# Kernel optimization log

Measured on AMD Instinct MI355X. Metric: run time of the kernel, lower is better.

Reference implementation:

```python
import jax, jax.numpy as jnp
import numpy as np

EXPR_MASK_RATIO = 0.4
POS_MASK_RATIO = 0.33
MIN_VISIBLE_GENES = 10


def setup_inputs() -> dict:
    key = jax.random.key(0)
    k1, k2 = jax.random.split(key)
    expression = jax.random.normal(k1, (16, 1024, 2000), dtype=jnp.float32)
    position = jax.random.normal(k2, (16, 1024, 3), dtype=jnp.float32)
    return {"expression": expression, "position": position}


def _expression_mask(expression, key):
    # strategy == 'random': rand matrix, kthvalue threshold, mask = rand >= threshold
    B, N, G = expression.shape
    num_masked = max(1, int(G * EXPR_MASK_RATIO))
    num_masked = min(num_masked, G - MIN_VISIBLE_GENES)
    rand = jax.random.uniform(key, (B, N, G), dtype=jnp.float32)
    # torch.kthvalue(rand, G - num_masked): (G - num_masked)-th smallest value,
    # i.e. index G - num_masked - 1 of the ascending sort (keepdim=True).
    kth = jnp.sort(rand, axis=-1)[..., G - num_masked - 1 : G - num_masked]  # (B,N,1)
    return rand >= kth  # bool (B,N,G); includes the threshold element, as in torch code


def _position_mask(position, key):
    # Vectorized form of the per-(b,n) loop:
    #   r < ratio*0.3      -> mask 2 of 3 dims (randperm(3)[:2] == complement of one uniform dim)
    #   ratio*0.3 <= r < ratio -> mask 1 uniform dim
    B, N, _ = position.shape
    kr, k1, k2 = jax.random.split(key, 3)
    r = jax.random.uniform(kr, (B, N), dtype=jnp.float32)
    two = r < POS_MASK_RATIO * 0.3
    one = (r < POS_MASK_RATIO) & (~two)
    dim1 = jax.random.randint(k1, (B, N), 0, 3)  # dim masked in the 1-dim branch
    excl = jax.random.randint(k2, (B, N), 0, 3)  # dim kept in the 2-dim branch
    eye = jnp.eye(3, dtype=bool)
    m1 = eye[dim1]        # (B,N,3) one-hot
    m2 = ~eye[excl]       # (B,N,3) two hot
    false3 = jnp.zeros((B, N, 3), dtype=bool)
    return jnp.where(two[..., None], m2, jnp.where(one[..., None], m1, false3))


def reference(expression, position):
    key = jax.random.key(42)
    ke, kp = jax.random.split(key)
    expr_mask = _expression_mask(expression, ke)   # (B,N,G) bool
    pos_mask = _position_mask(position, kp)        # (B,N,3) bool
    return expr_mask, pos_mask
```

## Files before the change

### kernel.cpp

```cpp
#include <hip/hip_runtime.h>
#include <stdint.h>

#define TF_ROUND(x0, x1, r)                    \
  {                                            \
    x0 += x1;                                  \
    x1 = (x1 << (r)) | (x1 >> (32 - (r)));     \
    x1 ^= x0;                                  \
  }

__host__ __device__ inline void threefry2x32(uint32_t k0, uint32_t k1,
                                             uint32_t x0, uint32_t x1,
                                             uint32_t& o0, uint32_t& o1) {
  const uint32_t ks2 = k0 ^ k1 ^ 0x1BD11BDAu;
  x0 += k0; x1 += k1;
  TF_ROUND(x0, x1, 13) TF_ROUND(x0, x1, 15) TF_ROUND(x0, x1, 26) TF_ROUND(x0, x1, 6)
  x0 += k1; x1 += ks2 + 1u;
  TF_ROUND(x0, x1, 17) TF_ROUND(x0, x1, 29) TF_ROUND(x0, x1, 16) TF_ROUND(x0, x1, 24)
  x0 += ks2; x1 += k0 + 2u;
  TF_ROUND(x0, x1, 13) TF_ROUND(x0, x1, 15) TF_ROUND(x0, x1, 26) TF_ROUND(x0, x1, 6)
  x0 += k0; x1 += k1 + 3u;
  TF_ROUND(x0, x1, 17) TF_ROUND(x0, x1, 29) TF_ROUND(x0, x1, 16) TF_ROUND(x0, x1, 24)
  x0 += k1; x1 += ks2 + 4u;
  TF_ROUND(x0, x1, 13) TF_ROUND(x0, x1, 15) TF_ROUND(x0, x1, 26) TF_ROUND(x0, x1, 6)
  x0 += ks2; x1 += k0 + 5u;
  o0 = x0; o1 = x1;
}

__device__ inline uint32_t random_bits32(uint32_t k0, uint32_t k1, uint32_t i) {
  uint32_t y0, y1;
  threefry2x32(k0, k1, 0u, i, y0, y1);
  return y0 ^ y1;
}

constexpr int B = 16;
constexpr int N = 1024;
constexpr int G = 2000;
constexpr int NUM_ROWS = B * N;
constexpr uint32_t RANK = (uint32_t)(G - 800 - 1);
constexpr long long EXPR_ELEMS = (long long)NUM_ROWS * G;
constexpr int PER_THREAD = 8;
constexpr int ACTIVE_T = G / PER_THREAD;

typedef int v4i __attribute__((ext_vector_type(4)));

__global__ __launch_bounds__(256) void fused_mask_kernel(
    int32_t* __restrict__ out_expr, int32_t* __restrict__ out_pos,
    uint32_t ke0, uint32_t ke1,
    uint32_t kr0, uint32_t kr1,
    uint32_t ah0, uint32_t ah1, uint32_t al0, uint32_t al1,
    uint32_t bh0, uint32_t bh1, uint32_t bl0, uint32_t bl1) {
  __shared__ alignas(16) uint32_t hist[256];
  __shared__ uint32_t cand[256];
  __shared__ uint32_t s_posbits[5];
  __shared__ uint32_t s_cnt;
  __shared__ uint32_t s_bucket;
  __shared__ uint32_t s_kk;
  __shared__ uint32_t s_thr;

  const int t = threadIdx.x;
  const uint32_t row = blockIdx.x;
  const uint32_t base = row * (uint32_t)G + (uint32_t)t * (uint32_t)PER_THREAD;
  const bool active = (t < ACTIVE_T);

  hist[t] = 0u;
  if (t == 0) s_cnt = 0u;
  __syncthreads();

  uint32_t m[PER_THREAD];
  if (active) {
#pragma unroll
    for (int j = 0; j < PER_THREAD; ++j) {
      uint32_t bits = random_bits32(ke0, ke1, base + (uint32_t)j);
      m[j] = bits >> 9;
      atomicAdd(&hist[m[j] >> 15], 1u);
    }
  } else if (t < 255) {
    uint32_t pk0, pk1;
    switch (t) {
      case 250: pk0 = kr0; pk1 = kr1; break;
      case 251: pk0 = ah0; pk1 = ah1; break;
      case 252: pk0 = al0; pk1 = al1; break;
      case 253: pk0 = bh0; pk1 = bh1; break;
      default:  pk0 = bl0; pk1 = bl1; break;
    }
    s_posbits[t - 250] = random_bits32(pk0, pk1, row);
  }
  __syncthreads();

  if (t < 64) {
    uint4 h = reinterpret_cast<const uint4*>(hist)[t];
    uint32_t tot = h.x + h.y + h.z + h.w;
    uint32_t x = tot;
#pragma unroll
    for (int d = 1; d < 64; d <<= 1) {
      uint32_t o = __shfl_up(x, d, 64);
      if (t >= d) x += o;
    }
    uint32_t e0 = x - tot;
    uint32_t e1 = e0 + h.x;
    uint32_t e2 = e1 + h.y;
    uint32_t e3 = e2 + h.z;
    if (e0 <= RANK && RANK < e1) { s_bucket = 4u * t + 0u; s_kk = RANK - e0; }
    if (e1 <= RANK && RANK < e2) { s_bucket = 4u * t + 1u; s_kk = RANK - e1; }
    if (e2 <= RANK && RANK < e3) { s_bucket = 4u * t + 2u; s_kk = RANK - e2; }
    if (e3 <= RANK && RANK < e3 + h.w) { s_bucket = 4u * t + 3u; s_kk = RANK - e3; }
  } else if (t == 255) {
    uint32_t rb = s_posbits[0];
    union { uint32_t u; float f; } cvt;
    cvt.u = (rb >> 9) | 0x3F800000u;
    float r = cvt.f - 1.0f;
    const float THR2 = (float)(0.33 * 0.3);
    const float THR1 = (float)0.33;
    bool two = r < THR2;
    bool one = (r < THR1) && !two;
    int dim1 = (int)(((s_posbits[1] % 3u) + (s_posbits[2] % 3u)) % 3u);
    int excl = (int)(((s_posbits[3] % 3u) + (s_posbits[4] % 3u)) % 3u);
    uint32_t obase = row * 3u;
#pragma unroll
    for (int d = 0; d < 3; ++d) {
      bool mval = two ? (d != excl) : (one ? (d == dim1) : false);
      out_pos[obase + (uint32_t)d] = mval ? 1 : 0;
    }
  }
  __syncthreads();

  const uint32_t bucket = s_bucket;
  if (active) {
#pragma unroll
    for (int j = 0; j < PER_THREAD; ++j) {
      if ((m[j] >> 15) == bucket) {
        uint32_t p = atomicAdd(&s_cnt, 1u);
        if (p < 256u) cand[p] = m[j];
      }
    }
  }
  __syncthreads();

  const uint32_t c = (s_cnt < 256u) ? s_cnt : 256u;
  const uint32_t kk = s_kk;
  if ((uint32_t)t < c) {
    uint32_t mv = cand[t];
    uint32_t r = 0;
    for (uint32_t j = 0; j < c; ++j) {
      uint32_t mj = cand[j];
      r += (mj < mv) || (mj == mv && j < (uint32_t)t);
    }
    if (r == kk) s_thr = mv;
  }
  __syncthreads();

  const uint32_t thr = s_thr;
  if (active) {
    v4i a, b;
    a.x = (m[0] >= thr) ? 1 : 0;
    a.y = (m[1] >= thr) ? 1 : 0;
    a.z = (m[2] >= thr) ? 1 : 0;
    a.w = (m[3] >= thr) ? 1 : 0;
    b.x = (m[4] >= thr) ? 1 : 0;
    b.y = (m[5] >= thr) ? 1 : 0;
    b.z = (m[6] >= thr) ? 1 : 0;
    b.w = (m[7] >= thr) ? 1 : 0;
    v4i* p = (v4i*)(out_expr + base);
    __builtin_nontemporal_store(a, p);
    __builtin_nontemporal_store(b, p + 1);
  }
}

extern "C" void kernel_launch(void* const* d_in, const int* in_sizes, int n_in,
                              void* d_out, int out_size, void* d_ws, size_t ws_size,
                              hipStream_t stream) {
  (void)d_in; (void)in_sizes; (void)n_in; (void)d_ws; (void)ws_size; (void)out_size;

  uint32_t ke0, ke1, kp0, kp1;
  threefry2x32(0u, 42u, 0u, 0u, ke0, ke1);
  threefry2x32(0u, 42u, 0u, 1u, kp0, kp1);
  uint32_t kr0, kr1, ka0, ka1, kb0, kb1;
  threefry2x32(kp0, kp1, 0u, 0u, kr0, kr1);
  threefry2x32(kp0, kp1, 0u, 1u, ka0, ka1);
  threefry2x32(kp0, kp1, 0u, 2u, kb0, kb1);
  uint32_t ah0, ah1, al0, al1, bh0, bh1, bl0, bl1;
  threefry2x32(ka0, ka1, 0u, 0u, ah0, ah1);
  threefry2x32(ka0, ka1, 0u, 1u, al0, al1);
  threefry2x32(kb0, kb1, 0u, 0u, bh0, bh1);
  threefry2x32(kb0, kb1, 0u, 1u, bl0, bl1);

  int32_t* out_expr = (int32_t*)d_out;
  int32_t* out_pos = out_expr + EXPR_ELEMS;

  fused_mask_kernel<<<NUM_ROWS, 256, 0, stream>>>(
      out_expr, out_pos, ke0, ke1, kr0, kr1,
      ah0, ah1, al0, al1, bh0, bh1, bl0, bl1);
}
```

Baseline: 244.1 us.

## Process one row per wavefront with wave-level selection and 4-wide threefry

Each 64-lane wavefront now handles a whole row, 32 elements per lane, so a block covers four rows. Block-wide __syncthreads are replaced with wave barriers, shuffles and ballots for the histogram scan, candidate ranking and threshold broadcast. Threefry is computed four counters at a time with alignbit rotates, and stores become coalesced 16-byte chunks strided by 256 elements. The cost is much higher register pressure from m[32], which may lower occupancy, and the candidate buffer is capped at 64 entries.

```diff
diff --git a/kernel.cpp b/kernel.cpp
--- a/kernel.cpp
+++ b/kernel.cpp
@@ -26,10 +26,34 @@
   o0 = x0; o1 = x1;
 }
 
-__device__ inline uint32_t random_bits32(uint32_t k0, uint32_t k1, uint32_t i) {
-  uint32_t y0, y1;
-  threefry2x32(k0, k1, 0u, i, y0, y1);
-  return y0 ^ y1;
+#define RND4(r)                                                     \
+  _Pragma("unroll") for (int e = 0; e < 4; ++e) {                   \
+    x0[e] += x1[e];                                                 \
+    x1[e] = __builtin_amdgcn_alignbit(x1[e], x1[e], 32u - (r));     \
+    x1[e] ^= x0[e];                                                 \
+  }
+#define INJ4(a, b)                                                  \
+  _Pragma("unroll") for (int e = 0; e < 4; ++e) {                   \
+    x0[e] += (a);                                                   \
+    x1[e] += (b);                                                   \
+  }
+
+__device__ __forceinline__ void tf4(uint32_t k0, uint32_t k1, uint32_t ks2,
+                                    uint32_t tbk, uint32_t lit, uint32_t out[4]) {
+  uint32_t x0[4], x1[4];
+#pragma unroll
+  for (int e = 0; e < 4; ++e) { x0[e] = k0; x1[e] = tbk + (lit + (uint32_t)e); }
+  RND4(13) RND4(15) RND4(26) RND4(6)
+  INJ4(k1, ks2 + 1u)
+  RND4(17) RND4(29) RND4(16) RND4(24)
+  INJ4(ks2, k0 + 2u)
+  RND4(13) RND4(15) RND4(26) RND4(6)
+  INJ4(k0, k1 + 3u)
+  RND4(17) RND4(29) RND4(16) RND4(24)
+  INJ4(k1, ks2 + 4u)
+  RND4(13) RND4(15) RND4(26) RND4(6)
+#pragma unroll
+  for (int e = 0; e < 4; ++e) out[e] = (x0[e] + ks2) ^ (x1[e] + (k0 + 5u));
 }
 
 constexpr int B = 16;
@@ -38,8 +62,7 @@
 constexpr int NUM_ROWS = B * N;
 constexpr uint32_t RANK = (uint32_t)(G - 800 - 1);
 constexpr long long EXPR_ELEMS = (long long)NUM_ROWS * G;
-constexpr int PER_THREAD = 8;
-constexpr int ACTIVE_T = G / PER_THREAD;
+constexpr int ROWS_PER_BLOCK = 4;
 
 typedef int v4i __attribute__((ext_vector_type(4)));
 
@@ -49,120 +72,149 @@
     uint32_t kr0, uint32_t kr1,
     uint32_t ah0, uint32_t ah1, uint32_t al0, uint32_t al1,
     uint32_t bh0, uint32_t bh1, uint32_t bl0, uint32_t bl1) {
-  __shared__ alignas(16) uint32_t hist[256];
-  __shared__ uint32_t cand[256];
-  __shared__ uint32_t s_posbits[5];
-  __shared__ uint32_t s_cnt;
-  __shared__ uint32_t s_bucket;
-  __shared__ uint32_t s_kk;
-  __shared__ uint32_t s_thr;
+  __shared__ alignas(16) uint32_t hist[ROWS_PER_BLOCK][256];
+  __shared__ uint32_t cand[ROWS_PER_BLOCK][64];
+  __shared__ uint32_t cnt[ROWS_PER_BLOCK];
 
   const int t = threadIdx.x;
-  const uint32_t row = blockIdx.x;
-  const uint32_t base = row * (uint32_t)G + (uint32_t)t * (uint32_t)PER_THREAD;
-  const bool active = (t < ACTIVE_T);
-
-  hist[t] = 0u;
-  if (t == 0) s_cnt = 0u;
-  __syncthreads();
-
-  uint32_t m[PER_THREAD];
-  if (active) {
-#pragma unroll
-    for (int j = 0; j < PER_THREAD; ++j) {
-      uint32_t bits = random_bits32(ke0, ke1, base + (uint32_t)j);
-      m[j] = bits >> 9;
-      atomicAdd(&hist[m[j] >> 15], 1u);
-    }
-  } else if (t < 255) {
-    uint32_t pk0, pk1;
-    switch (t) {
-      case 250: pk0 = kr0; pk1 = kr1; break;
-      case 251: pk0 = ah0; pk1 = ah1; break;
-      case 252: pk0 = al0; pk1 = al1; break;
-      case 253: pk0 = bh0; pk1 = bh1; break;
-      default:  pk0 = bl0; pk1 = bl1; break;
-    }
-    s_posbits[t - 250] = random_bits32(pk0, pk1, row);
-  }
-  __syncthreads();
-
-  if (t < 64) {
-    uint4 h = reinterpret_cast<const uint4*>(hist)[t];
-    uint32_t tot = h.x + h.y + h.z + h.w;
-    uint32_t x = tot;
-#pragma unroll
-    for (int d = 1; d < 64; d <<= 1) {
-      uint32_t o = __shfl_up(x, d, 64);
-      if (t >= d) x += o;
-    }
-    uint32_t e0 = x - tot;
-    uint32_t e1 = e0 + h.x;
-    uint32_t e2 = e1 + h.y;
-    uint32_t e3 = e2 + h.z;
-    if (e0 <= RANK && RANK < e1) { s_bucket = 4u * t + 0u; s_kk = RANK - e0; }
-    if (e1 <= RANK && RANK < e2) { s_bucket = 4u * t + 1u; s_kk = RANK - e1; }
-    if (e2 <= RANK && RANK < e3) { s_bucket = 4u * t + 2u; s_kk = RANK - e2; }
-    if (e3 <= RANK && RANK < e3 + h.w) { s_bucket = 4u * t + 3u; s_kk = RANK - e3; }
-  } else if (t == 255) {
-    uint32_t rb = s_posbits[0];
-    union { uint32_t u; float f; } cvt;
-    cvt.u = (rb >> 9) | 0x3F800000u;
-    float r = cvt.f - 1.0f;
-    const float THR2 = (float)(0.33 * 0.3);
-    const float THR1 = (float)0.33;
-    bool two = r < THR2;
-    bool one = (r < THR1) && !two;
-    int dim1 = (int)(((s_posbits[1] % 3u) + (s_posbits[2] % 3u)) % 3u);
-    int excl = (int)(((s_posbits[3] % 3u) + (s_posbits[4] % 3u)) % 3u);
-    uint32_t obase = row * 3u;
-#pragma unroll
-    for (int d = 0; d < 3; ++d) {
-      bool mval = two ? (d != excl) : (one ? (d == dim1) : false);
-      out_pos[obase + (uint32_t)d] = mval ? 1 : 0;
-    }
-  }
-  __syncthreads();
-
-  const uint32_t bucket = s_bucket;
-  if (active) {
-#pragma unroll
-    for (int j = 0; j < PER_THREAD; ++j) {
-      if ((m[j] >> 15) == bucket) {
-        uint32_t p = atomicAdd(&s_cnt, 1u);
-        if (p < 256u) cand[p] = m[j];
+  const int lane = t & 63;
+  const int w = t >> 6;
+  const uint32_t row = blockIdx.x * (uint32_t)ROWS_PER_BLOCK + (uint32_t)w;
+  const uint32_t rbase = row * (uint32_t)G;
+
+  {
+    uint4 z = make_uint4(0u, 0u, 0u, 0u);
+    *reinterpret_cast<uint4*>(&hist[w][lane * 4]) = z;
+  }
+  if (lane == 0) cnt[w] = 0u;
+  __builtin_amdgcn_wave_barrier();
+
+  const uint32_t ks2 = ke0 ^ ke1 ^ 0x1BD11BDAu;
+  const uint32_t tbk = rbase + (uint32_t)(lane << 2) + ke1;
+
+  uint32_t m[32];
+  uint32_t pb = 0u;
+
+#pragma unroll
+  for (int j = 0; j < 7; ++j) {
+    uint32_t o[4];
+    tf4(ke0, ke1, ks2, tbk, (uint32_t)(j * 256), o);
+#pragma unroll
+    for (int e = 0; e < 4; ++e) {
+      m[j * 4 + e] = o[e] >> 9;
+      atomicAdd(&hist[w][o[e] >> 24], 1u);
+    }
+  }
+  if (lane < 52) {
+    uint32_t o[4];
+    tf4(ke0, ke1, ks2, tbk, 1792u, o);
+#pragma unroll
+    for (int e = 0; e < 4; ++e) {
+      m[28 + e] = o[e] >> 9;
+      atomicAdd(&hist[w][o[e] >> 24], 1u);
+    }
+  } else {
+#pragma unroll
+    for (int e = 0; e < 4; ++e) m[28 + e] = 0xFFFFFFFFu;
+    if (lane < 57) {
+      uint32_t pk0, pk1;
+      switch (lane) {
+        case 52: pk0 = kr0; pk1 = kr1; break;
+        case 53: pk0 = ah0; pk1 = ah1; break;
+        case 54: pk0 = al0; pk1 = al1; break;
+        case 55: pk0 = bh0; pk1 = bh1; break;
+        default: pk0 = bl0; pk1 = bl1; break;
       }
-    }
-  }
-  __syncthreads();
-
-  const uint32_t c = (s_cnt < 256u) ? s_cnt : 256u;
-  const uint32_t kk = s_kk;
-  if ((uint32_t)t < c) {
-    uint32_t mv = cand[t];
-    uint32_t r = 0;
-    for (uint32_t j = 0; j < c; ++j) {
-      uint32_t mj = cand[j];
-      r += (mj < mv) || (mj == mv && j < (uint32_t)t);
-    }
-    if (r == kk) s_thr = mv;
-  }
-  __syncthreads();
-
-  const uint32_t thr = s_thr;
-  if (active) {
-    v4i a, b;
-    a.x = (m[0] >= thr) ? 1 : 0;
-    a.y = (m[1] >= thr) ? 1 : 0;
-    a.z = (m[2] >= thr) ? 1 : 0;
-    a.w = (m[3] >= thr) ? 1 : 0;
-    b.x = (m[4] >= thr) ? 1 : 0;
-    b.y = (m[5] >= thr) ? 1 : 0;
-    b.z = (m[6] >= thr) ? 1 : 0;
-    b.w = (m[7] >= thr) ? 1 : 0;
-    v4i* p = (v4i*)(out_expr + base);
-    __builtin_nontemporal_store(a, p);
-    __builtin_nontemporal_store(b, p + 1);
+      uint32_t y0, y1;
+      threefry2x32(pk0, pk1, 0u, row, y0, y1);
+      pb = y0 ^ y1;
+    }
+  }
+  __builtin_amdgcn_wave_barrier();
+
+  uint4 h = *reinterpret_cast<const uint4*>(&hist[w][lane * 4]);
+  uint32_t tot = h.x + h.y + h.z + h.w;
+  uint32_t x = tot;
+#pragma unroll
+  for (int d = 1; d < 64; d <<= 1) {
+    uint32_t o = __shfl_up(x, d, 64);
+    if (lane >= d) x += o;
+  }
+  const uint32_t e0 = x - tot;
+  bool found = (e0 <= RANK) && (RANK < x);
+  uint32_t bl_ = 0u, kl = 0u;
+  if (found) {
+    uint32_t e1 = e0 + h.x, e2 = e1 + h.y, e3 = e2 + h.z;
+    if (RANK < e1)      { bl_ = 4u * lane + 0u; kl = RANK - e0; }
+    else if (RANK < e2) { bl_ = 4u * lane + 1u; kl = RANK - e1; }
+    else if (RANK < e3) { bl_ = 4u * lane + 2u; kl = RANK - e2; }
+    else                { bl_ = 4u * lane + 3u; kl = RANK - e3; }
+  }
+  unsigned long long bm = __ballot(found);
+  const int src = __builtin_ctzll(bm);
+  const uint32_t bucket = (uint32_t)__shfl((int)bl_, src, 64);
+  const uint32_t kk = (uint32_t)__shfl((int)kl, src, 64);
+
+#pragma unroll
+  for (int i = 0; i < 32; ++i) {
+    if ((m[i] >> 15) == bucket) {
+      uint32_t p = atomicAdd(&cnt[w], 1u);
+      if (p < 64u) cand[w][p] = m[i];
+    }
+  }
+  __builtin_amdgcn_wave_barrier();
+
+  uint32_t c = cnt[w];
+  c = (uint32_t)__builtin_amdgcn_readfirstlane((int)c);
+  if (c > 64u) c = 64u;
+  uint32_t myc = cand[w][lane];
+  uint32_t r = 0u;
+  for (uint32_t j = 0; j < c; ++j) {
+    uint32_t vj = (uint32_t)__shfl((int)myc, (int)j, 64);
+    r += (vj < myc || (vj == myc && j < (uint32_t)lane)) ? 1u : 0u;
+  }
+  bool win = ((uint32_t)lane < c) && (r == kk);
+  unsigned long long wm = __ballot(win);
+  const uint32_t thr = (uint32_t)__shfl((int)myc, __builtin_ctzll(wm), 64);
+
+  {
+    uint32_t p0 = (uint32_t)__shfl((int)pb, 52, 64);
+    uint32_t p1 = (uint32_t)__shfl((int)pb, 53, 64);
+    uint32_t p2 = (uint32_t)__shfl((int)pb, 54, 64);
+    uint32_t p3 = (uint32_t)__shfl((int)pb, 55, 64);
+    uint32_t p4 = (uint32_t)__shfl((int)pb, 56, 64);
+    if (lane < 3) {
+      union { uint32_t u; float f; } cvt;
+      cvt.u = (p0 >> 9) | 0x3F800000u;
+      float rr = cvt.f - 1.0f;
+      const float THR2 = (float)(0.33 * 0.3);
+      const float THR1 = (float)0.33;
+      bool two = rr < THR2;
+      bool one = (rr < THR1) && !two;
+      int dim1 = (int)(((p1 % 3u) + (p2 % 3u)) % 3u);
+      int excl = (int)(((p3 % 3u) + (p4 % 3u)) % 3u);
+      bool mval = two ? (lane != excl) : (one ? (lane == dim1) : false);
+      out_pos[row * 3u + (uint32_t)lane] = mval ? 1 : 0;
+    }
+  }
+
+  int32_t* op = out_expr + rbase + (uint32_t)(lane << 2);
+#pragma unroll
+  for (int j = 0; j < 7; ++j) {
+    v4i a;
+    a.x = (m[j * 4 + 0] >= thr) ? 1 : 0;
+    a.y = (m[j * 4 + 1] >= thr) ? 1 : 0;
+    a.z = (m[j * 4 + 2] >= thr) ? 1 : 0;
+    a.w = (m[j * 4 + 3] >= thr) ? 1 : 0;
+    __builtin_nontemporal_store(a, (v4i*)(op + j * 256));
+  }
+  if (lane < 52) {
+    v4i a;
+    a.x = (m[28] >= thr) ? 1 : 0;
+    a.y = (m[29] >= thr) ? 1 : 0;
+    a.z = (m[30] >= thr) ? 1 : 0;
+    a.w = (m[31] >= thr) ? 1 : 0;
+    __builtin_nontemporal_store(a, (v4i*)(op + 1792));
   }
 }
 
@@ -187,7 +239,7 @@
   int32_t* out_expr = (int32_t*)d_out;
   int32_t* out_pos = out_expr + EXPR_ELEMS;
 
-  fused_mask_kernel<<<NUM_ROWS, 256, 0, stream>>>(
+  fused_mask_kernel<<<NUM_ROWS / ROWS_PER_BLOCK, 256, 0, stream>>>(
       out_expr, out_pos, ke0, ke1, kr0, kr1,
       ah0, ah1, al0, al1, bh0, bh1, bl0, bl1);
 }
```

Result: no change. 244.5 us (+0.1%).
